# Optimization experiments

Hardware: AMD Instinct MI355X
Metric: run time of the kernel (lower is better)

The kernel has to match this reference:

```python
import jax, jax.numpy as jnp
import numpy as np

HEADS, DIM_HEAD, DIM = 12, 64, 768
H = W = 32
N = H * W
B = 4


def _ln(x, g, b, eps=1e-5):
    mu = x.mean(-1, keepdims=True)
    var = ((x - mu) ** 2).mean(-1, keepdims=True)
    return (x - mu) / jnp.sqrt(var + eps) * g + b


def _get_epipolar(k, src_c2w, target_c2w, h=H, w=W):
    # Faithful port of Epipolar_Attention.get_epipolar, without the (hw*hw,3) repeat
    # materialization (uses broadcasting for the pairwise cross product instead).
    b = k.shape[0]
    Wf = h * 16.0 / 9.0
    k = k.astype(jnp.float32)
    k = k.at[:, 0, :].multiply(Wf).at[:, 1, :].multiply(float(h))
    k = k.at[:, 0, 2].set(h / 2.0).at[:, 1, 2].set(h / 2.0)
    ii, jj = jnp.meshgrid(jnp.arange(h), jnp.arange(w), indexing='ij')
    # after the torch column swap: (col, row, 1)
    coords = jnp.stack([jj.ravel(), ii.ravel(), jnp.ones(h * w, jnp.int32)], axis=1).astype(jnp.float32)  # [hw,3]
    k3 = k[:, :3, :3]
    src_r, src_t = src_c2w[:, :3, :3].astype(jnp.float32), src_c2w[:, :3, 3].astype(jnp.float32)
    tgt_r, tgt_t = target_c2w[:, :3, :3].astype(jnp.float32), target_c2w[:, :3, 3].astype(jnp.float32)
    tgt_rinv = jnp.linalg.inv(tgt_r)
    fx, fy = k3[:, 0, 0][:, None], k3[:, 1, 1][:, None]
    cx, cy = k3[:, 0, 2][:, None], k3[:, 1, 2][:, None]
    nc = jnp.stack([(coords[None, :, 0] - cx) / fx,
                    (coords[None, :, 1] - cy) / fy,
                    jnp.broadcast_to(coords[None, :, 2], (b, h * w))], axis=-1)  # [b,hw,3]
    p3w = jnp.einsum('bij,bnj->bni', src_r, nc) + src_t[:, None]
    p2 = jnp.einsum('bij,bnj->bni', tgt_rinv, p3w) - tgt_t[:, None]  # target_w2c_t = -target_c2w_t
    pij_un = jnp.einsum('bij,bnj->bni', k3, p2)                      # [b,hw,3]
    pij = pij_un / (pij_un[..., -1:] + 1e-6)
    o2 = jnp.einsum('bij,bj->bi', tgt_rinv, src_t) - tgt_t           # origin projected
    oij = jnp.einsum('bij,bj->bi', k3, o2)
    oij = oij / oij[..., -1:]
    oi_to_pi = pij - oij[:, None]                # [b,hw,3]
    oi_to_coord = coords[None] - oij[:, None]    # [b,hw,3]
    cr = jnp.cross(oi_to_pi[:, :, None, :], oi_to_coord[:, None, :, :])  # [b,hw,hw,3]
    area = jnp.sqrt((cr * cr).sum(-1))
    vlen = jnp.sqrt((oi_to_pi * oi_to_pi).sum(-1))[:, :, None]
    dist = area / vlen
    dw = 1.0 - jax.nn.sigmoid(50.0 * (dist - 0.5))
    row_max = dw.max(-1, keepdims=True)
    return jnp.where(row_max < 0.5, 1.0, dw)     # rows with max<0.5 are set to all-ones


def setup_inputs():
    key = jax.random.key(0)
    ks = jax.random.split(key, 16)
    s = 0.02
    x = jax.random.normal(ks[0], (B, N, DIM), jnp.float32)
    src_encode = jax.random.normal(ks[1], (B, N, DIM), jnp.float32)
    intrinsic = (jnp.zeros((B, 4, 4), jnp.float32)
                 .at[:, 0, 0].set(1.0).at[:, 1, 1].set(1.0)
                 .at[:, 0, 2].set(0.5).at[:, 1, 2].set(0.5)
                 .at[:, 2, 2].set(1.0).at[:, 3, 3].set(1.0))
    R = jnp.eye(3, dtype=jnp.float32) + 0.1 * jax.random.normal(ks[2], (2, B, 3, 3), jnp.float32)
    t = 0.5 * jax.random.normal(ks[3], (2, B, 3), jnp.float32)
    c2w = (jnp.zeros((2, B, 4, 4), jnp.float32)
           .at[:, :, :3, :3].set(R).at[:, :, :3, 3].set(t).at[:, :, 3, 3].set(1.0))
    hd = HEADS * DIM_HEAD
    w_ = lambda k_, shp: s * jax.random.normal(k_, shp, jnp.float32)
    return dict(
        x=x, src_encode=src_encode, intrinsic=intrinsic, c2w=c2w,
        lnq_g=jnp.ones(DIM), lnq_b=jnp.zeros(DIM), Wq=w_(ks[4], (DIM, hd)), bq=jnp.zeros(hd),
        lnk_g=jnp.ones(DIM), lnk_b=jnp.zeros(DIM), Wk=w_(ks[5], (DIM, hd)), bk=jnp.zeros(hd),
        lnv_g=jnp.ones(DIM), lnv_b=jnp.zeros(DIM), Wv=w_(ks[6], (DIM, hd)), bv=jnp.zeros(hd),
        Wp=w_(ks[7], (hd, DIM)), bp=jnp.zeros(DIM),
        pre_g=jnp.ones(DIM), pre_b=jnp.zeros(DIM),
        W1=w_(ks[8], (DIM, 2 * DIM)), b1=jnp.zeros(2 * DIM),
        W2=w_(ks[9], (2 * DIM, DIM)), b2=jnp.zeros(DIM),
        post_g=jnp.ones(DIM), post_b=jnp.zeros(DIM))


def reference(x, src_encode, intrinsic, c2w, lnq_g, lnq_b, Wq, bq, lnk_g, lnk_b, Wk, bk,
              lnv_g, lnv_b, Wv, bv, Wp, bp, pre_g, pre_b, W1, b1, W2, b2, post_g, post_b):
    b, n, _ = x.shape
    scale = DIM_HEAD ** -0.5
    split = lambda t_: t_.reshape(b, n, HEADS, DIM_HEAD).transpose(0, 2, 1, 3)  # [b,m,n,d]
    q = split(_ln(x, lnq_g, lnq_b) @ Wq + bq)
    k = split(_ln(src_encode, lnk_g, lnk_b) @ Wk + bk)
    v = split(_ln(src_encode, lnv_g, lnv_b) @ Wv + bv)
    scores = scale * jnp.einsum('bmqd,bmkd->bmqk', q, k)
    e1 = _get_epipolar(intrinsic, c2w[1], c2w[0])                    # do_epipolar
    e2 = jnp.swapaxes(_get_epipolar(intrinsic, c2w[0], c2w[1]), 1, 2)  # bidirectional (transposed)
    wmap = e1 * e2                                                   # [b,n,n], shared across heads
    att = jax.nn.softmax(scores * wmap[:, None], axis=-1)
    a = jnp.einsum('bmqk,bmkd->bmqd', att, v).transpose(0, 2, 1, 3).reshape(b, n, HEADS * DIM_HEAD)
    z = _ln(a @ Wp + bp, pre_g, pre_b)
    z = z + (jax.nn.gelu(z @ W1 + b1, approximate=False) @ W2 + b2)  # torch nn.GELU = exact erf
    z = _ln(z, post_g, post_b)
    wm_full = jnp.broadcast_to(wmap[:, None], (b, HEADS, n, n)).reshape(b * HEADS, n, n)
    return z, wm_full
```

## Files before the change

kernel.cpp:

```cpp
#include <hip/hip_runtime.h>
#include <hip/hip_bf16.h>

typedef unsigned short u16;
typedef __attribute__((ext_vector_type(4))) unsigned short u16x4;
typedef __attribute__((ext_vector_type(8))) unsigned short u16x8;
typedef __attribute__((ext_vector_type(8))) short s16x8;
typedef __attribute__((ext_vector_type(4))) float f32x4;

#define HEADS 12
#define NSEQ 1024
#define DIMM 768
#define DHEAD 64

__device__ __forceinline__ float b2f(u16 h) {
  union { unsigned u; float f; } v; v.u = ((unsigned)h) << 16; return v.f;
}
__device__ __forceinline__ u16 f2b(float f) {
  union { float f; unsigned u; } v; v.f = f;
  unsigned r = v.u + 0x7fffu + ((v.u >> 16) & 1u);
  return (u16)(r >> 16);
}
__device__ __forceinline__ void gl_lds16(const u16* g, u16* l) {
  __builtin_amdgcn_global_load_lds(
      (const __attribute__((address_space(1))) void*)g,
      (__attribute__((address_space(3))) void*)l, 16, 0, 0);
}

template<bool GELU, bool RESID>
__device__ __forceinline__ void gemm_body(
    const u16* __restrict__ A, const u16* __restrict__ BT,
    const float* __restrict__ bias, const u16* __restrict__ resid,
    const float* __restrict__ rg, const float* __restrict__ rb,
    u16* __restrict__ C, int K, int lda, int ldb, int ldc,
    int m0, int n0, u16* As, u16* Bs)
{
  const int tid = threadIdx.x;
  const int lane = tid & 63;
  const int wv = tid >> 6;
  const int wm0 = (wv >> 1) * 64;
  const int wn0 = (wv & 1) * 64;
  const int l15 = lane & 15;
  const int quad = lane >> 4;
  const int srow = lane >> 2;
  const int scol = (lane & 3) * 8;

  f32x4 acc[4][4];
  #pragma unroll
  for (int i = 0; i < 4; ++i)
    #pragma unroll
    for (int j = 0; j < 4; ++j)
      acc[i][j] = {0.f, 0.f, 0.f, 0.f};

  const u16* Ab = A + (long)(m0 + wv * 32 + srow) * lda + scol;
  const u16* Bb = BT + (long)(n0 + wv * 32 + srow) * ldb + scol;
  u16* AsW = As + (wv * 32) * 32;
  u16* BsW = Bs + (wv * 32) * 32;

  #pragma unroll
  for (int t = 0; t < 2; ++t) {
    gl_lds16(Ab + (long)t * 16 * lda, AsW + t * 16 * 32);
    gl_lds16(Bb + (long)t * 16 * ldb, BsW + t * 16 * 32);
  }

  int cur = 0;
  for (int k0 = 0; k0 < K; k0 += 32) {
    __syncthreads();
    if (k0 + 32 < K) {
      const int nxt = cur ^ 1;
      #pragma unroll
      for (int t = 0; t < 2; ++t) {
        gl_lds16(Ab + (k0 + 32) + (long)t * 16 * lda, AsW + nxt * 4096 + t * 16 * 32);
        gl_lds16(Bb + (k0 + 32) + (long)t * 16 * ldb, BsW + nxt * 4096 + t * 16 * 32);
      }
    }
    const u16* Ac = As + cur * 4096;
    const u16* Bc = Bs + cur * 4096;
    s16x8 af[4], bfr[4];
    #pragma unroll
    for (int i = 0; i < 4; ++i)
      af[i] = *(const s16x8*)&Ac[(wm0 + i * 16 + l15) * 32 + quad * 8];
    #pragma unroll
    for (int j = 0; j < 4; ++j)
      bfr[j] = *(const s16x8*)&Bc[(wn0 + j * 16 + l15) * 32 + quad * 8];
    #pragma unroll
    for (int i = 0; i < 4; ++i)
      #pragma unroll
      for (int j = 0; j < 4; ++j)
        acc[i][j] = __builtin_amdgcn_mfma_f32_16x16x32_bf16(af[i], bfr[j], acc[i][j], 0, 0, 0);
    cur ^= 1;
  }

  #pragma unroll
  for (int i = 0; i < 4; ++i)
    #pragma unroll
    for (int j = 0; j < 4; ++j) {
      const int col = n0 + wn0 + j * 16 + l15;
      const float bvv = bias[col];
      #pragma unroll
      for (int v = 0; v < 4; ++v) {
        const int row = m0 + wm0 + i * 16 + quad * 4 + v;
        float val = acc[i][j][v] + bvv;
        if (GELU) val = 0.5f * val * (1.0f + erff(val * 0.70710678118654752440f));
        if (RESID) val += b2f(resid[(long)row * ldc + col]) * rg[col] + rb[col];
        C[(long)row * ldc + col] = f2b(val);
      }
    }
}

template<bool GELU, bool RESID>
__device__ __forceinline__ void gemm_body64(
    const u16* __restrict__ A, const u16* __restrict__ BT,
    const float* __restrict__ bias, const u16* __restrict__ resid,
    const float* __restrict__ rg, const float* __restrict__ rb,
    u16* __restrict__ C, int K, int lda, int ldb, int ldc,
    int m0, int n0, u16* As, u16* Bs)
{
  const int tid = threadIdx.x;
  const int lane = tid & 63;
  const int wv = tid >> 6;
  const int wm0 = wv * 32;
  const int l15 = lane & 15;
  const int quad = lane >> 4;
  const int srow = lane >> 2;
  const int scol = (lane & 3) * 8;

  f32x4 acc[2][4];
  #pragma unroll
  for (int i = 0; i < 2; ++i)
    #pragma unroll
    for (int j = 0; j < 4; ++j)
      acc[i][j] = {0.f, 0.f, 0.f, 0.f};

  const u16* Ab = A + (long)(m0 + wv * 32 + srow) * lda + scol;
  const u16* Bb = BT + (long)(n0 + wv * 16 + srow) * ldb + scol;
  u16* AsW = As + (wv * 32) * 32;
  u16* BsW = Bs + (wv * 16) * 32;

  #pragma unroll
  for (int t = 0; t < 2; ++t)
    gl_lds16(Ab + (long)t * 16 * lda, AsW + t * 16 * 32);
  gl_lds16(Bb, BsW);

  int cur = 0;
  for (int k0 = 0; k0 < K; k0 += 32) {
    __syncthreads();
    if (k0 + 32 < K) {
      const int nxt = cur ^ 1;
      #pragma unroll
      for (int t = 0; t < 2; ++t)
        gl_lds16(Ab + (k0 + 32) + (long)t * 16 * lda, AsW + nxt * 4096 + t * 16 * 32);
      gl_lds16(Bb + (k0 + 32), BsW + nxt * 2048);
    }
    const u16* Ac = As + cur * 4096;
    const u16* Bc = Bs + cur * 2048;
    s16x8 af[2], bfr[4];
    #pragma unroll
    for (int i = 0; i < 2; ++i)
      af[i] = *(const s16x8*)&Ac[(wm0 + i * 16 + l15) * 32 + quad * 8];
    #pragma unroll
    for (int j = 0; j < 4; ++j)
      bfr[j] = *(const s16x8*)&Bc[(j * 16 + l15) * 32 + quad * 8];
    #pragma unroll
    for (int i = 0; i < 2; ++i)
      #pragma unroll
      for (int j = 0; j < 4; ++j)
        acc[i][j] = __builtin_amdgcn_mfma_f32_16x16x32_bf16(af[i], bfr[j], acc[i][j], 0, 0, 0);
    cur ^= 1;
  }

  #pragma unroll
  for (int i = 0; i < 2; ++i)
    #pragma unroll
    for (int j = 0; j < 4; ++j) {
      const int col = n0 + j * 16 + l15;
      const float bvv = bias[col];
      #pragma unroll
      for (int v = 0; v < 4; ++v) {
        const int row = m0 + wm0 + i * 16 + quad * 4 + v;
        float val = acc[i][j][v] + bvv;
        if (GELU) val = 0.5f * val * (1.0f + erff(val * 0.70710678118654752440f));
        if (RESID) val += b2f(resid[(long)row * ldc + col]) * rg[col] + rb[col];
        C[(long)row * ldc + col] = f2b(val);
      }
    }
}

template<bool GELU, bool RESID>
__global__ __launch_bounds__(256)
void gemm_one(const u16* __restrict__ A, const u16* __restrict__ BT,
              const float* __restrict__ bias, const u16* __restrict__ resid,
              const float* __restrict__ rg, const float* __restrict__ rb,
              u16* __restrict__ C, int K, int lda, int ldb, int ldc)
{
  __shared__ u16 As[8192], Bs[4096];
  gemm_body64<GELU, RESID>(A, BT, bias, resid, rg, rb, C, K, lda, ldb, ldc,
                           blockIdx.x * 128, blockIdx.y * 64, As, Bs);
}

__global__ __launch_bounds__(256)
void gemm_qkv(const u16* __restrict__ nx, const u16* __restrict__ ns,
              const u16* __restrict__ qT, const u16* __restrict__ kvT,
              const float* __restrict__ bqf, const float* __restrict__ bkvf,
              u16* __restrict__ qb, u16* __restrict__ kvb)
{
  __shared__ u16 As[8192], Bs[8192];
  const int z = blockIdx.z;
  if (z == 0)
    gemm_body<false, false>(nx, qT, bqf, nullptr, nullptr, nullptr, qb,
                            768, 768, 768, 768,
                            blockIdx.x * 128, blockIdx.y * 128, As, Bs);
  else
    gemm_body<false, false>(ns, kvT, bkvf, nullptr, nullptr, nullptr, kvb,
                            768, 768, 768, 1536,
                            blockIdx.x * 128, (z - 1) * 768 + blockIdx.y * 128, As, Bs);
}

__global__ __launch_bounds__(256, 3)
void fattn(const u16* __restrict__ qb, const u16* __restrict__ kvb,
           const u16* __restrict__ vT, const u16* __restrict__ wm,
           u16* __restrict__ outA)
{
  __shared__ u16 Qs[2 * 64 * 32];
  __shared__ u16 Ks[2][2 * 64 * 32];
  __shared__ u16 Vs[2][2 * 64 * 32];
  __shared__ u16 Ps[64][72];

  const int bh = blockIdx.y;
  const int b = bh / HEADS, h = bh - b * HEADS;
  const int q0 = blockIdx.x * 64;
  const int tid = threadIdx.x;
  const int lane = tid & 63;
  const int wv = tid >> 6;
  const int l15 = lane & 15;
  const int quad = lane >> 4;
  const int srow = lane >> 2;
  const int scol = (lane & 3) * 8;

  const u16* Qg = qb + ((long)b * NSEQ + q0) * DIMM + h * DHEAD;
  const u16* Kg = kvb + (long)b * NSEQ * 1536 + h * DHEAD;
  const u16* Vg = vT + (long)bh * DHEAD * NSEQ;
  const u16* Wg = wm + ((long)b * NSEQ + q0) * NSEQ;

  #pragma unroll
  for (int h2 = 0; h2 < 2; ++h2) {
    gl_lds16(Qg + (long)(wv * 16 + srow) * DIMM + h2 * 32 + scol,
             Qs + (h2 * 64 + wv * 16) * 32);
    gl_lds16(Kg + (long)(wv * 16 + srow) * 1536 + h2 * 32 + scol,
             Ks[0] + (h2 * 64 + wv * 16) * 32);
    gl_lds16(Vg + (long)(wv * 16 + srow) * NSEQ + h2 * 32 + scol,
             Vs[0] + (h2 * 64 + wv * 16) * 32);
  }

  f32x4 Sacc[4], Oacc[4];
  float mrow[4], lrow[4];
  #pragma unroll
  for (int j = 0; j < 4; ++j) {
    Oacc[j] = {0.f, 0.f, 0.f, 0.f};
    mrow[j] = -3.0e38f;
    lrow[j] = 0.f;
  }
  s16x8 qf[2];

  int cur = 0;
  for (int kt = 0; kt < 16; ++kt) {
    __syncthreads();
    if (kt < 15) {
      const int nxt = cur ^ 1;
      #pragma unroll
      for (int h2 = 0; h2 < 2; ++h2) {
        gl_lds16(Kg + (long)((kt + 1) * 64 + wv * 16 + srow) * 1536 + h2 * 32 + scol,
                 Ks[nxt] + (h2 * 64 + wv * 16) * 32);
        gl_lds16(Vg + (long)(wv * 16 + srow) * NSEQ + (kt + 1) * 64 + h2 * 32 + scol,
                 Vs[nxt] + (h2 * 64 + wv * 16) * 32);
      }
    }

    if (kt == 0) {
      qf[0] = *(const s16x8*)&Qs[(0 * 64 + wv * 16 + l15) * 32 + quad * 8];
      qf[1] = *(const s16x8*)&Qs[(1 * 64 + wv * 16 + l15) * 32 + quad * 8];
    }

    float wr[4][4];
    #pragma unroll
    for (int j = 0; j < 4; ++j)
      #pragma unroll
      for (int v = 0; v < 4; ++v)
        wr[j][v] = b2f(Wg[(long)(wv * 16 + quad * 4 + v) * NSEQ + kt * 64 + j * 16 + l15]);

    #pragma unroll
    for (int j = 0; j < 4; ++j) Sacc[j] = {0.f, 0.f, 0.f, 0.f};
    #pragma unroll
    for (int j = 0; j < 4; ++j)
      #pragma unroll
      for (int h2 = 0; h2 < 2; ++h2) {
        s16x8 kf = *(const s16x8*)&Ks[cur][(h2 * 64 + j * 16 + l15) * 32 + quad * 8];
        Sacc[j] = __builtin_amdgcn_mfma_f32_16x16x32_bf16(qf[h2], kf, Sacc[j], 0, 0, 0);
      }

    #pragma unroll
    for (int j = 0; j < 4; ++j)
      #pragma unroll
      for (int v = 0; v < 4; ++v)
        Sacc[j][v] *= wr[j][v];
    #pragma unroll
    for (int v = 0; v < 4; ++v) {
      float tm = fmaxf(fmaxf(Sacc[0][v], Sacc[1][v]), fmaxf(Sacc[2][v], Sacc[3][v]));
      tm = fmaxf(tm, __shfl_xor(tm, 1));
      tm = fmaxf(tm, __shfl_xor(tm, 2));
      tm = fmaxf(tm, __shfl_xor(tm, 4));
      tm = fmaxf(tm, __shfl_xor(tm, 8));
      const float mnew = fmaxf(mrow[v], tm);
      const float al = __expf(mrow[v] - mnew);
      float rs = 0.f;
      #pragma unroll
      for (int j = 0; j < 4; ++j) {
        const float e = __expf(Sacc[j][v] - mnew);
        Sacc[j][v] = e;
        rs += e;
      }
      rs += __shfl_xor(rs, 1);
      rs += __shfl_xor(rs, 2);
      rs += __shfl_xor(rs, 4);
      rs += __shfl_xor(rs, 8);
      lrow[v] = lrow[v] * al + rs;
      mrow[v] = mnew;
      #pragma unroll
      for (int jn = 0; jn < 4; ++jn) Oacc[jn][v] *= al;
    }
    #pragma unroll
    for (int j = 0; j < 4; ++j)
      #pragma unroll
      for (int v = 0; v < 4; ++v)
        Ps[wv * 16 + quad * 4 + v][j * 16 + l15] = f2b(Sacc[j][v]);

    #pragma unroll
    for (int h2 = 0; h2 < 2; ++h2) {
      s16x8 af = *(const s16x8*)&Ps[wv * 16 + l15][h2 * 32 + quad * 8];
      #pragma unroll
      for (int jn = 0; jn < 4; ++jn) {
        s16x8 vf = *(const s16x8*)&Vs[cur][(h2 * 64 + jn * 16 + l15) * 32 + quad * 8];
        Oacc[jn] = __builtin_amdgcn_mfma_f32_16x16x32_bf16(af, vf, Oacc[jn], 0, 0, 0);
      }
    }
    cur ^= 1;
  }

  #pragma unroll
  for (int v = 0; v < 4; ++v) {
    const int row = q0 + wv * 16 + quad * 4 + v;
    const float inv = 1.0f / lrow[v];
    #pragma unroll
    for (int jn = 0; jn < 4; ++jn)
      outA[((long)(b * NSEQ + row)) * DIMM + h * DHEAD + jn * 16 + l15] =
          f2b(Oacc[jn][v] * inv);
  }
}

template<bool F32IN>
__global__ __launch_bounds__(256)
void norm_k(const void* __restrict__ in, u16* __restrict__ out)
{
  const long base = (long)blockIdx.x * DIMM;
  const int tid = threadIdx.x;
  __shared__ float s1[8], s2[8];
  float v0, v1, v2;
  if (F32IN) {
    const float* p = (const float*)in + base;
    v0 = p[tid]; v1 = p[tid + 256]; v2 = p[tid + 512];
  } else {
    const u16* p = (const u16*)in + base;
    v0 = b2f(p[tid]); v1 = b2f(p[tid + 256]); v2 = b2f(p[tid + 512]);
  }
  float s = v0 + v1 + v2;
  #pragma unroll
  for (int off = 32; off; off >>= 1) s += __shfl_down(s, off);
  const int lane = tid & 63, wid = tid >> 6;
  if (!lane) s1[wid] = s;
  __syncthreads();
  if (!tid) s1[4] = s1[0] + s1[1] + s1[2] + s1[3];
  __syncthreads();
  const float mu = s1[4] / 768.0f;
  float d0 = v0 - mu, d1 = v1 - mu, d2 = v2 - mu;
  float sq = d0 * d0 + d1 * d1 + d2 * d2;
  #pragma unroll
  for (int off = 32; off; off >>= 1) sq += __shfl_down(sq, off);
  if (!lane) s2[wid] = sq;
  __syncthreads();
  if (!tid) s2[4] = s2[0] + s2[1] + s2[2] + s2[3];
  __syncthreads();
  const float rstd = 1.0f / sqrtf(s2[4] / 768.0f + 1e-5f);
  u16* o = out + base;
  o[tid]       = f2b(d0 * rstd);
  o[tid + 256] = f2b(d1 * rstd);
  o[tid + 512] = f2b(d2 * rstd);
}

__global__ __launch_bounds__(256)
void norm_dual(const float* __restrict__ inA, const float* __restrict__ inB,
               u16* __restrict__ outA, u16* __restrict__ outB)
{
  const int r = blockIdx.x;
  const float* p = ((r < 4096) ? inA : inB) + (long)(r & 4095) * DIMM;
  u16* o = ((r < 4096) ? outA : outB) + (long)(r & 4095) * DIMM;
  const int tid = threadIdx.x;
  __shared__ float s1[8], s2[8];
  float v0 = p[tid], v1 = p[tid + 256], v2 = p[tid + 512];
  float s = v0 + v1 + v2;
  #pragma unroll
  for (int off = 32; off; off >>= 1) s += __shfl_down(s, off);
  const int lane = tid & 63, wid = tid >> 6;
  if (!lane) s1[wid] = s;
  __syncthreads();
  if (!tid) s1[4] = s1[0] + s1[1] + s1[2] + s1[3];
  __syncthreads();
  const float mu = s1[4] / 768.0f;
  float d0 = v0 - mu, d1 = v1 - mu, d2 = v2 - mu;
  float sq = d0 * d0 + d1 * d1 + d2 * d2;
  #pragma unroll
  for (int off = 32; off; off >>= 1) sq += __shfl_down(sq, off);
  if (!lane) s2[wid] = sq;
  __syncthreads();
  if (!tid) s2[4] = s2[0] + s2[1] + s2[2] + s2[3];
  __syncthreads();
  const float rstd = 1.0f / sqrtf(s2[4] / 768.0f + 1e-5f);
  o[tid]       = f2b(d0 * rstd);
  o[tid + 256] = f2b(d1 * rstd);
  o[tid + 512] = f2b(d2 * rstd);
}

__global__ __launch_bounds__(256)
void ln_final(const u16* __restrict__ in, const float* __restrict__ g,
              const float* __restrict__ bb, float* __restrict__ out)
{
  const long base = (long)blockIdx.x * DIMM;
  const int tid = threadIdx.x;
  __shared__ float s1[8], s2[8];
  const u16* p = in + base;
  float v0 = b2f(p[tid]), v1 = b2f(p[tid + 256]), v2 = b2f(p[tid + 512]);
  float s = v0 + v1 + v2;
  #pragma unroll
  for (int off = 32; off; off >>= 1) s += __shfl_down(s, off);
  const int lane = tid & 63, wid = tid >> 6;
  if (!lane) s1[wid] = s;
  __syncthreads();
  if (!tid) s1[4] = s1[0] + s1[1] + s1[2] + s1[3];
  __syncthreads();
  const float mu = s1[4] / 768.0f;
  float d0 = v0 - mu, d1 = v1 - mu, d2 = v2 - mu;
  float sq = d0 * d0 + d1 * d1 + d2 * d2;
  #pragma unroll
  for (int off = 32; off; off >>= 1) sq += __shfl_down(sq, off);
  if (!lane) s2[wid] = sq;
  __syncthreads();
  if (!tid) s2[4] = s2[0] + s2[1] + s2[2] + s2[3];
  __syncthreads();
  const float rstd = 1.0f / sqrtf(s2[4] / 768.0f + 1e-5f);
  float* o = out + base;
  o[tid]       = d0 * rstd * g[tid]       + bb[tid];
  o[tid + 256] = d1 * rstd * g[tid + 256] + bb[tid + 256];
  o[tid + 512] = d2 * rstd * g[tid + 512] + bb[tid + 512];
}

__global__ __launch_bounds__(256)
void trans_all(const float* w0, const float* w1, const float* w2,
               const float* w3, const float* w4, const float* w5,
               const float* gq, const float* gk, const float* gv, const float* gp,
               u16* d0, u16* d12, u16* d3, u16* d4, u16* d5)
{
  const float* src; const float* g; u16* dst; int R, C; float sc = 1.0f;
  switch (blockIdx.z) {
    case 0: src = w0; g = gq; dst = d0;  R = 768;  C = 768;  sc = 0.125f; break;
    case 1: src = w1; g = gk; dst = d12; R = 768;  C = 768;  break;
    case 2: src = w2; g = gv; dst = d12 + 768 * 768; R = 768; C = 768; break;
    case 3: src = w3; g = nullptr; dst = d3; R = 768;  C = 768;  break;
    case 4: src = w4; g = gp; dst = d4; R = 768;  C = 1536; break;
    default: src = w5; g = nullptr; dst = d5; R = 1536; C = 768; break;
  }
  const int c0 = blockIdx.x * 32;
  const int r0 = blockIdx.y * 32;
  if (c0 >= C || r0 >= R) return;
  __shared__ u16 t[32][36];
  const int tid = threadIdx.x;
  const int i = tid >> 3;
  const int j4 = (tid & 7) * 4;
  const float rs = (g ? g[r0 + i] : 1.0f) * sc;
  #pragma unroll
  for (int jj = 0; jj < 4; ++jj)
    t[i][j4 + jj] = f2b(src[(long)(r0 + i) * C + c0 + j4 + jj] * rs);
  __syncthreads();
  u16x4 ov;
  #pragma unroll
  for (int jj = 0; jj < 4; ++jj) ov[jj] = t[j4 + jj][i];
  *(u16x4*)&dst[(long)(c0 + i) * R + r0 + j4] = ov;
}

__global__ __launch_bounds__(256)
void biasfold(const float* Wq, const float* Wk, const float* Wv, const float* W1,
              const float* bq, const float* bk, const float* bv, const float* b1,
              const float* lnqb, const float* lnkb, const float* lnvb, const float* preb,
              float* obq, float* obkv, float* ob1)
{
  const int y = blockIdx.y;
  const int c = blockIdx.x * 256 + threadIdx.x;
  const float* W; const float* bln; const float* bw; float* out;
  int C; float sc = 1.0f;
  switch (y) {
    case 0: W = Wq; bln = lnqb; bw = bq; out = obq;        C = 768;  sc = 0.125f; break;
    case 1: W = Wk; bln = lnkb; bw = bk; out = obkv;       C = 768;  break;
    case 2: W = Wv; bln = lnvb; bw = bv; out = obkv + 768; C = 768;  break;
    default: W = W1; bln = preb; bw = b1; out = ob1;       C = 1536; break;
  }
  if (c >= C) return;
  float s = bw[c];
  for (int r = 0; r < 768; ++r) s += bln[r] * W[(long)r * C + c];
  out[c] = s * sc;
}

__global__ __launch_bounds__(256)
void v_transpose(const u16* __restrict__ kvb, u16* __restrict__ vT)
{
  __shared__ u16 t[64][72];
  const int z = blockIdx.y;
  const int b = z / HEADS, h = z - b * HEADS;
  const int n0 = blockIdx.x * 64;
  const int tid = threadIdx.x;
  const int i = tid >> 2;
  const int jb = (tid & 3) * 16;
  const u16* src = kvb + (long)(b * NSEQ + n0 + i) * 1536 + 768 + h * DHEAD + jb;
  *(u16x8*)&t[i][jb]     = *(const u16x8*)&src[0];
  *(u16x8*)&t[i][jb + 8] = *(const u16x8*)&src[8];
  __syncthreads();
  const int dd = tid >> 2;
  const int nb = (tid & 3) * 16;
  u16x8 o0, o1;
  #pragma unroll
  for (int nn = 0; nn < 8; ++nn) { o0[nn] = t[nb + nn][dd]; o1[nn] = t[nb + 8 + nn][dd]; }
  u16* dst = vT + ((long)z * DHEAD + dd) * NSEQ + n0 + nb;
  *(u16x8*)&dst[0] = o0;
  *(u16x8*)&dst[8] = o1;
}

__global__ void epi_setup(const float* __restrict__ intr, const float* __restrict__ c2w,
                          float* __restrict__ u4, float* __restrict__ oijb)
{
  const int db = blockIdx.x;
  const int d = db >> 2, b = db & 3;
  __shared__ float S[36];
  if (threadIdx.x == 0) {
    const int sidx = (d == 0) ? 1 : 0;
    const int tidx = 1 - sidx;
    float k3[9], sr[9], st[3], tr[9], tt[3];
    const float Wf = 32.0f * 16.0f / 9.0f;
    for (int j = 0; j < 3; ++j) {
      k3[j]     = intr[(b * 4 + 0) * 4 + j] * Wf;
      k3[3 + j] = intr[(b * 4 + 1) * 4 + j] * 32.0f;
      k3[6 + j] = intr[(b * 4 + 2) * 4 + j];
    }
    k3[2] = 16.0f; k3[5] = 16.0f;
    for (int i = 0; i < 3; ++i) {
      for (int j = 0; j < 3; ++j) {
        sr[i * 3 + j] = c2w[((sidx * 4 + b) * 4 + i) * 4 + j];
        tr[i * 3 + j] = c2w[((tidx * 4 + b) * 4 + i) * 4 + j];
      }
      st[i] = c2w[((sidx * 4 + b) * 4 + i) * 4 + 3];
      tt[i] = c2w[((tidx * 4 + b) * 4 + i) * 4 + 3];
    }
    double a = tr[0], bb_ = tr[1], c = tr[2];
    double dd2 = tr[3], e = tr[4], f = tr[5];
    double g2 = tr[6], h2 = tr[7], i2 = tr[8];
    double det = a * (e * i2 - f * h2) - bb_ * (dd2 * i2 - f * g2) + c * (dd2 * h2 - e * g2);
    double inv[9] = {
      (e * i2 - f * h2), (c * h2 - bb_ * i2), (bb_ * f - c * e),
      (f * g2 - dd2 * i2), (a * i2 - c * g2), (c * dd2 - a * f),
      (dd2 * h2 - e * g2), (bb_ * g2 - a * h2), (a * e - bb_ * dd2)
    };
    float tri[9];
    for (int t2 = 0; t2 < 9; ++t2) tri[t2] = (float)(inv[t2] / det);
    float o2[3], oij[3];
    for (int i3 = 0; i3 < 3; ++i3)
      o2[i3] = tri[i3 * 3] * st[0] + tri[i3 * 3 + 1] * st[1] + tri[i3 * 3 + 2] * st[2] - tt[i3];
    for (int i3 = 0; i3 < 3; ++i3)
      oij[i3] = k3[i3 * 3] * o2[0] + k3[i3 * 3 + 1] * o2[1] + k3[i3 * 3 + 2] * o2[2];
    const float ozf = oij[2];
    oij[0] = oij[0] / ozf; oij[1] = oij[1] / ozf; oij[2] = ozf / ozf;
    for (int t2 = 0; t2 < 9; ++t2) { S[t2] = k3[t2]; S[9 + t2] = sr[t2]; S[21 + t2] = tri[t2]; }
    for (int t2 = 0; t2 < 3; ++t2) { S[18 + t2] = st[t2]; S[30 + t2] = tt[t2]; S[33 + t2] = oij[t2]; }
    oijb[db * 4 + 0] = oij[0]; oijb[db * 4 + 1] = oij[1]; oijb[db * 4 + 2] = oij[2];
    oijb[db * 4 + 3] = 0.f;
  }
  __syncthreads();
  for (int n = threadIdx.x; n < 1024; n += blockDim.x) {
    const float ncx = ((float)(n & 31) - S[2]) / S[0];
    const float ncy = ((float)(n >> 5) - S[5]) / S[4];
    const float p0 = S[9]  * ncx + S[10] * ncy + S[11] + S[18];
    const float p1 = S[12] * ncx + S[13] * ncy + S[14] + S[19];
    const float p2 = S[15] * ncx + S[16] * ncy + S[17] + S[20];
    const float q0 = S[21] * p0 + S[22] * p1 + S[23] * p2 - S[30];
    const float q1 = S[24] * p0 + S[25] * p1 + S[26] * p2 - S[31];
    const float q2 = S[27] * p0 + S[28] * p1 + S[29] * p2 - S[32];
    const float w0 = S[0] * q0 + S[1] * q1 + S[2] * q2;
    const float w1 = S[3] * q0 + S[4] * q1 + S[5] * q2;
    const float w2 = S[6] * q0 + S[7] * q1 + S[8] * q2;
    const float pz = w2 + 1e-6f;
    const float ux = w0 / pz - S[33];
    const float uy = w1 / pz - S[34];
    const float uz = w2 / pz - S[35];
    const float vlen = sqrtf(ux * ux + uy * uy + uz * uz);
    f32x4 uo = {ux, uy, uz, vlen};
    *(f32x4*)&u4[((long)db * 1024 + n) * 4] = uo;
  }
}

__device__ __forceinline__ float dwval(f32x4 U, float ox, float oy, float oz, int m)
{
  const float cx = (float)(m & 31) - ox;
  const float cy = (float)(m >> 5) - oy;
  const float cz = 1.0f - oz;
  const float crx = U.y * cz - U.z * cy;
  const float cry = U.z * cx - U.x * cz;
  const float crz = U.x * cy - U.y * cx;
  const float area = sqrtf(crx * crx + cry * cry + crz * crz);
  const float dist = area / U.w;
  const float t = 50.0f * (dist - 0.5f);
  return 1.0f - 1.0f / (1.0f + __expf(-t));
}

__global__ __launch_bounds__(256)
void epi_flags(const float* __restrict__ u4, const float* __restrict__ oijb,
               float* __restrict__ flags)
{
  const int rowid = blockIdx.x;
  const int db = rowid >> 10;
  const f32x4 U = *(const f32x4*)&u4[(long)rowid * 4];
  const float ox = oijb[db * 4 + 0];
  const float oy = oijb[db * 4 + 1];
  const float oz = oijb[db * 4 + 2];
  const int tid = threadIdx.x;
  __shared__ float red[8];
  float mx = -1e30f;
  #pragma unroll
  for (int i = 0; i < 4; ++i)
    mx = fmaxf(mx, dwval(U, ox, oy, oz, tid + i * 256));
  #pragma unroll
  for (int off = 32; off; off >>= 1) mx = fmaxf(mx, __shfl_down(mx, off));
  const int lane = tid & 63, wid = tid >> 6;
  if (!lane) red[wid] = mx;
  __syncthreads();
  if (!tid) {
    const float m4 = fmaxf(fmaxf(red[0], red[1]), fmaxf(red[2], red[3]));
    flags[rowid] = (m4 < 0.5f) ? 1.0f : 0.0f;
  }
}

__global__ __launch_bounds__(256)
void epi_wmap(const float* __restrict__ u4, const float* __restrict__ oijb,
              const float* __restrict__ flags,
              u16* __restrict__ wm, float* __restrict__ wm_full)
{
  const int b = blockIdx.z;
  const int q0 = blockIdx.x * 32;
  const int k0 = blockIdx.y * 32;
  const int tid = threadIdx.x;
  const int i = tid >> 3;
  const int j4 = (tid & 7) * 4;

  __shared__ f32x4 U2s[32];
  __shared__ float f2s[32];
  __shared__ float f1s[32];
  if (tid < 32) {
    U2s[tid] = *(const f32x4*)&u4[((long)(4 + b) * 1024 + k0 + tid) * 4];
    f2s[tid] = flags[(4 + b) * 1024 + k0 + tid];
    f1s[tid] = flags[b * 1024 + q0 + tid];
  }
  __syncthreads();

  const int q = q0 + i;
  const f32x4 U1 = *(const f32x4*)&u4[((long)b * 1024 + q) * 4];
  const float o1x = oijb[b * 4 + 0], o1y = oijb[b * 4 + 1], o1z = oijb[b * 4 + 2];
  const float o2x = oijb[(4 + b) * 4 + 0], o2y = oijb[(4 + b) * 4 + 1], o2z = oijb[(4 + b) * 4 + 2];
  const bool fl1 = f1s[i] > 0.5f;

  u16x4 pk;
  f32x4 wf;
  #pragma unroll
  for (int jj = 0; jj < 4; ++jj) {
    const int k = k0 + j4 + jj;
    const float e1 = fl1 ? 1.0f : dwval(U1, o1x, o1y, o1z, k);
    const float e2 = (f2s[j4 + jj] > 0.5f) ? 1.0f : dwval(U2s[j4 + jj], o2x, o2y, o2z, q);
    const float w = e1 * e2;
    wf[jj] = w;
    pk[jj] = f2b(w);
  }
  *(u16x4*)&wm[((long)b * 1024 + q0 + i) * 1024 + k0 + j4] = pk;
  #pragma unroll
  for (int h = 0; h < HEADS; ++h)
    *(f32x4*)&wm_full[((long)(b * HEADS + h) * 1024 + q0 + i) * 1024 + k0 + j4] = wf;
}

extern "C" void kernel_launch(void* const* d_in, const int* in_sizes, int n_in,
                              void* d_out, int out_size, void* d_ws, size_t ws_size,
                              hipStream_t stream)
{
  (void)in_sizes; (void)n_in; (void)out_size; (void)ws_size;
  const float* x     = (const float*)d_in[0];
  const float* src   = (const float*)d_in[1];
  const float* intr  = (const float*)d_in[2];
  const float* c2w   = (const float*)d_in[3];
  const float* lnq_g = (const float*)d_in[4];
  const float* lnq_b = (const float*)d_in[5];
  const float* Wq    = (const float*)d_in[6];
  const float* bq    = (const float*)d_in[7];
  const float* lnk_g = (const float*)d_in[8];
  const float* lnk_b = (const float*)d_in[9];
  const float* Wk    = (const float*)d_in[10];
  const float* bk    = (const float*)d_in[11];
  const float* lnv_g = (const float*)d_in[12];
  const float* lnv_b = (const float*)d_in[13];
  const float* Wv    = (const float*)d_in[14];
  const float* bv    = (const float*)d_in[15];
  const float* Wp    = (const float*)d_in[16];
  const float* bp    = (const float*)d_in[17];
  const float* pre_g = (const float*)d_in[18];
  const float* pre_b = (const float*)d_in[19];
  const float* W1    = (const float*)d_in[20];
  const float* b1    = (const float*)d_in[21];
  const float* W2    = (const float*)d_in[22];
  const float* b2    = (const float*)d_in[23];
  const float* post_g= (const float*)d_in[24];
  const float* post_b= (const float*)d_in[25];

  char* ws = (char*)d_ws;
  size_t off = 0;
  auto alloc = [&](size_t bytes) -> char* {
    char* p = ws + off;
    off = (off + bytes + 255) & ~(size_t)255;
    return p;
  };
  const size_t SEQD = (size_t)4096 * 768 * 2;

  u16* WqT  = (u16*)alloc(768 * 768 * 2);
  u16* WkvT = (u16*)alloc((size_t)1536 * 768 * 2);
  u16* WpT  = (u16*)alloc(768 * 768 * 2);
  u16* W1T  = (u16*)alloc(768 * 1536 * 2);
  u16* W2T  = (u16*)alloc(1536 * 768 * 2);
  float* bqf  = (float*)alloc(768 * 4);
  float* bkvf = (float*)alloc(1536 * 4);
  float* b1f  = (float*)alloc(1536 * 4);
  char* pool = alloc(6 * SEQD);
  float* u4   = (float*)alloc(8 * 1024 * 4 * 4);
  float* oijb = (float*)alloc(8 * 4 * 4);
  u16* wmapb  = (u16*)alloc((size_t)4 * 1024 * 1024 * 2);
  float* flagb = (float*)alloc(8 * 1024 * 4);

  u16* S0 = (u16*)pool;
  u16* S1 = (u16*)(pool + SEQD);
  u16* S2 = (u16*)(pool + 2 * SEQD);
  u16* S3 = (u16*)(pool + 3 * SEQD);
  u16* S5 = (u16*)(pool + 5 * SEQD);

  float* out_z  = (float*)d_out;
  float* out_wm = (float*)d_out + (size_t)4 * 1024 * 768;

  trans_all<<<dim3(48, 48, 6), 256, 0, stream>>>(
      Wq, Wk, Wv, Wp, W1, W2, lnq_g, lnk_g, lnv_g, pre_g,
      WqT, WkvT, WpT, W1T, W2T);
  biasfold<<<dim3(6, 4), 256, 0, stream>>>(
      Wq, Wk, Wv, W1, bq, bk, bv, b1, lnq_b, lnk_b, lnv_b, pre_b,
      bqf, bkvf, b1f);

  epi_setup<<<8, 128, 0, stream>>>(intr, c2w, u4, oijb);
  epi_flags<<<8192, 256, 0, stream>>>(u4, oijb, flagb);
  epi_wmap<<<dim3(32, 32, 4), 256, 0, stream>>>(u4, oijb, flagb, wmapb, out_wm);

  norm_dual<<<8192, 256, 0, stream>>>(x, src, S0, S1);

  gemm_qkv<<<dim3(32, 6, 3), 256, 0, stream>>>(S0, S1, WqT, WkvT, bqf, bkvf, S2, S3);

  v_transpose<<<dim3(16, 48), 256, 0, stream>>>(S3, S5);

  fattn<<<dim3(16, 48), 256, 0, stream>>>(S2, S3, S5, wmapb, S0);

  gemm_one<false, false><<<dim3(32, 12), 256, 0, stream>>>(
      S0, WpT, bp, nullptr, nullptr, nullptr, S1, 768, 768, 768, 768);

  norm_k<false><<<4096, 256, 0, stream>>>(S1, S2);

  gemm_one<true, false><<<dim3(32, 24), 256, 0, stream>>>(
      S2, W1T, b1f, nullptr, nullptr, nullptr, S3, 768, 768, 768, 1536);

  gemm_one<false, true><<<dim3(32, 12), 256, 0, stream>>>(
      S3, W2T, b2, S2, pre_g, pre_b, S5, 1536, 1536, 1536, 768);

  ln_final<<<4096, 256, 0, stream>>>(S5, post_g, post_b, out_z);
}
```

Measured before the change: 518.7 us.

## Triple-buffer GEMM LDS loads with vmcnt waits and fuse biasfold into weight prep

Both GEMM bodies move from double to triple buffering of LDS tiles filled by direct global-to-LDS loads. Each iteration waits with explicit s_waitcnt vmcnt counts and a raw barrier instead of __syncthreads, so two tiles stay in flight and load latency is hidden better. Separately, the bias-folding kernel is merged into the weight transpose kernel as an extra z-slice, with the 768-row reduction split over 8 thread groups, removing one launch and widening that reduction. The change raises LDS per block and depends on the hand-written vmcnt values matching the number of outstanding loads.

After: 511.5 us. About the same (-1.4%).

```diff
diff --git a/kernel.cpp b/kernel.cpp
--- a/kernel.cpp
+++ b/kernel.cpp
@@ -56,38 +56,43 @@
   u16* AsW = As + (wv * 32) * 32;
   u16* BsW = Bs + (wv * 32) * 32;
 
-  #pragma unroll
-  for (int t = 0; t < 2; ++t) {
-    gl_lds16(Ab + (long)t * 16 * lda, AsW + t * 16 * 32);
-    gl_lds16(Bb + (long)t * 16 * ldb, BsW + t * 16 * 32);
-  }
+  auto issue = [&](int buf, int kk) {
+    #pragma unroll
+    for (int t = 0; t < 2; ++t) {
+      gl_lds16(Ab + kk + (long)t * 16 * lda, AsW + buf * 4096 + t * 16 * 32);
+      gl_lds16(Bb + kk + (long)t * 16 * ldb, BsW + buf * 4096 + t * 16 * 32);
+    }
+  };
+
+  const int NK = K >> 5;
+  issue(0, 0);
+  issue(1, 32);
 
   int cur = 0;
-  for (int k0 = 0; k0 < K; k0 += 32) {
-    __syncthreads();
-    if (k0 + 32 < K) {
-      const int nxt = cur ^ 1;
-      #pragma unroll
-      for (int t = 0; t < 2; ++t) {
-        gl_lds16(Ab + (k0 + 32) + (long)t * 16 * lda, AsW + nxt * 4096 + t * 16 * 32);
-        gl_lds16(Bb + (k0 + 32) + (long)t * 16 * ldb, BsW + nxt * 4096 + t * 16 * 32);
-      }
+  for (int i = 0; i < NK; ++i) {
+    if (i + 1 < NK) asm volatile("s_waitcnt vmcnt(4)" ::: "memory");
+    else            asm volatile("s_waitcnt vmcnt(0)" ::: "memory");
+    __builtin_amdgcn_s_barrier();
+    __builtin_amdgcn_sched_barrier(0);
+    if (i + 2 < NK) {
+      int nb = cur + 2; if (nb >= 3) nb -= 3;
+      issue(nb, (i + 2) * 32);
     }
     const u16* Ac = As + cur * 4096;
     const u16* Bc = Bs + cur * 4096;
     s16x8 af[4], bfr[4];
     #pragma unroll
-    for (int i = 0; i < 4; ++i)
-      af[i] = *(const s16x8*)&Ac[(wm0 + i * 16 + l15) * 32 + quad * 8];
+    for (int i2 = 0; i2 < 4; ++i2)
+      af[i2] = *(const s16x8*)&Ac[(wm0 + i2 * 16 + l15) * 32 + quad * 8];
     #pragma unroll
     for (int j = 0; j < 4; ++j)
       bfr[j] = *(const s16x8*)&Bc[(wn0 + j * 16 + l15) * 32 + quad * 8];
     #pragma unroll
-    for (int i = 0; i < 4; ++i)
+    for (int i2 = 0; i2 < 4; ++i2)
       #pragma unroll
       for (int j = 0; j < 4; ++j)
-        acc[i][j] = __builtin_amdgcn_mfma_f32_16x16x32_bf16(af[i], bfr[j], acc[i][j], 0, 0, 0);
-    cur ^= 1;
+        acc[i2][j] = __builtin_amdgcn_mfma_f32_16x16x32_bf16(af[i2], bfr[j], acc[i2][j], 0, 0, 0);
+    ++cur; if (cur == 3) cur = 0;
   }
 
   #pragma unroll
@@ -136,36 +141,42 @@
   u16* AsW = As + (wv * 32) * 32;
   u16* BsW = Bs + (wv * 16) * 32;
 
-  #pragma unroll
-  for (int t = 0; t < 2; ++t)
-    gl_lds16(Ab + (long)t * 16 * lda, AsW + t * 16 * 32);
-  gl_lds16(Bb, BsW);
+  auto issue = [&](int buf, int kk) {
+    #pragma unroll
+    for (int t = 0; t < 2; ++t)
+      gl_lds16(Ab + kk + (long)t * 16 * lda, AsW + buf * 4096 + t * 16 * 32);
+    gl_lds16(Bb + kk, BsW + buf * 2048);
+  };
+
+  const int NK = K >> 5;
+  issue(0, 0);
+  issue(1, 32);
 
   int cur = 0;
-  for (int k0 = 0; k0 < K; k0 += 32) {
-    __syncthreads();
-    if (k0 + 32 < K) {
-      const int nxt = cur ^ 1;
-      #pragma unroll
-      for (int t = 0; t < 2; ++t)
-        gl_lds16(Ab + (k0 + 32) + (long)t * 16 * lda, AsW + nxt * 4096 + t * 16 * 32);
-      gl_lds16(Bb + (k0 + 32), BsW + nxt * 2048);
+  for (int i = 0; i < NK; ++i) {
+    if (i + 1 < NK) asm volatile("s_waitcnt vmcnt(3)" ::: "memory");
+    else            asm volatile("s_waitcnt vmcnt(0)" ::: "memory");
+    __builtin_amdgcn_s_barrier();
+    __builtin_amdgcn_sched_barrier(0);
+    if (i + 2 < NK) {
+      int nb = cur + 2; if (nb >= 3) nb -= 3;
+      issue(nb, (i + 2) * 32);
     }
     const u16* Ac = As + cur * 4096;
     const u16* Bc = Bs + cur * 2048;
     s16x8 af[2], bfr[4];
     #pragma unroll
-    for (int i = 0; i < 2; ++i)
-      af[i] = *(const s16x8*)&Ac[(wm0 + i * 16 + l15) * 32 + quad * 8];
+    for (int i2 = 0; i2 < 2; ++i2)
+      af[i2] = *(const s16x8*)&Ac[(wm0 + i2 * 16 + l15) * 32 + quad * 8];
     #pragma unroll
     for (int j = 0; j < 4; ++j)
       bfr[j] = *(const s16x8*)&Bc[(j * 16 + l15) * 32 + quad * 8];
     #pragma unroll
-    for (int i = 0; i < 2; ++i)
+    for (int i2 = 0; i2 < 2; ++i2)
       #pragma unroll
       for (int j = 0; j < 4; ++j)
-        acc[i][j] = __builtin_amdgcn_mfma_f32_16x16x32_bf16(af[i], bfr[j], acc[i][j], 0, 0, 0);
-    cur ^= 1;
+        acc[i2][j] = __builtin_amdgcn_mfma_f32_16x16x32_bf16(af[i2], bfr[j], acc[i2][j], 0, 0, 0);
+    ++cur; if (cur == 3) cur = 0;
   }
 
   #pragma unroll
@@ -192,7 +203,7 @@
               const float* __restrict__ rg, const float* __restrict__ rb,
               u16* __restrict__ C, int K, int lda, int ldb, int ldc)
 {
-  __shared__ u16 As[8192], Bs[4096];
+  __shared__ u16 As[12288], Bs[6144];
   gemm_body64<GELU, RESID>(A, BT, bias, resid, rg, rb, C, K, lda, ldb, ldc,
                            blockIdx.x * 128, blockIdx.y * 64, As, Bs);
 }
@@ -203,7 +214,7 @@
               const float* __restrict__ bqf, const float* __restrict__ bkvf,
               u16* __restrict__ qb, u16* __restrict__ kvb)
 {
-  __shared__ u16 As[8192], Bs[8192];
+  __shared__ u16 As[12288], Bs[12288];
   const int z = blockIdx.z;
   if (z == 0)
     gemm_body<false, false>(nx, qT, bqf, nullptr, nullptr, nullptr, qb,
@@ -462,11 +473,48 @@
 }
 
 __global__ __launch_bounds__(256)
-void trans_all(const float* w0, const float* w1, const float* w2,
-               const float* w3, const float* w4, const float* w5,
-               const float* gq, const float* gk, const float* gv, const float* gp,
-               u16* d0, u16* d12, u16* d3, u16* d4, u16* d5)
-{
+void prep_all(const float* w0, const float* w1, const float* w2,
+              const float* w3, const float* w4, const float* w5,
+              const float* gq, const float* gk, const float* gv, const float* gp,
+              u16* d0, u16* d12, u16* d3, u16* d4, u16* d5,
+              const float* bq, const float* bk, const float* bv, const float* b1,
+              const float* lnqb, const float* lnkb, const float* lnvb, const float* preb,
+              float* obq, float* obkv, float* ob1)
+{
+  __shared__ u16 t[32][36];
+  __shared__ float red[8][32];
+  const int tid = threadIdx.x;
+
+  if (blockIdx.z == 6) {
+    const int y = blockIdx.y;
+    if (y >= 4) return;
+    const float* W; const float* bln; const float* bw; float* out;
+    int C; float sc = 1.0f;
+    switch (y) {
+      case 0: W = w0; bln = lnqb; bw = bq; out = obq;        C = 768;  sc = 0.125f; break;
+      case 1: W = w1; bln = lnkb; bw = bk; out = obkv;       C = 768;  break;
+      case 2: W = w2; bln = lnvb; bw = bv; out = obkv + 768; C = 768;  break;
+      default: W = w4; bln = preb; bw = b1; out = ob1;       C = 1536; break;
+    }
+    const int c0 = blockIdx.x * 32;
+    if (c0 >= C) return;
+    const int cl = tid & 31;
+    const int rg = tid >> 5;
+    const int c = c0 + cl;
+    float s = 0.f;
+    for (int r = rg * 96; r < rg * 96 + 96; ++r)
+      s += bln[r] * W[(long)r * C + c];
+    red[rg][cl] = s;
+    __syncthreads();
+    if (rg == 0) {
+      float tot = bw[c];
+      #pragma unroll
+      for (int k = 0; k < 8; ++k) tot += red[k][cl];
+      out[c] = tot * sc;
+    }
+    return;
+  }
+
   const float* src; const float* g; u16* dst; int R, C; float sc = 1.0f;
   switch (blockIdx.z) {
     case 0: src = w0; g = gq; dst = d0;  R = 768;  C = 768;  sc = 0.125f; break;
@@ -479,8 +527,6 @@
   const int c0 = blockIdx.x * 32;
   const int r0 = blockIdx.y * 32;
   if (c0 >= C || r0 >= R) return;
-  __shared__ u16 t[32][36];
-  const int tid = threadIdx.x;
   const int i = tid >> 3;
   const int j4 = (tid & 7) * 4;
   const float rs = (g ? g[r0 + i] : 1.0f) * sc;
@@ -492,28 +538,6 @@
   #pragma unroll
   for (int jj = 0; jj < 4; ++jj) ov[jj] = t[j4 + jj][i];
   *(u16x4*)&dst[(long)(c0 + i) * R + r0 + j4] = ov;
-}
-
-__global__ __launch_bounds__(256)
-void biasfold(const float* Wq, const float* Wk, const float* Wv, const float* W1,
-              const float* bq, const float* bk, const float* bv, const float* b1,
-              const float* lnqb, const float* lnkb, const float* lnvb, const float* preb,
-              float* obq, float* obkv, float* ob1)
-{
-  const int y = blockIdx.y;
-  const int c = blockIdx.x * 256 + threadIdx.x;
-  const float* W; const float* bln; const float* bw; float* out;
-  int C; float sc = 1.0f;
-  switch (y) {
-    case 0: W = Wq; bln = lnqb; bw = bq; out = obq;        C = 768;  sc = 0.125f; break;
-    case 1: W = Wk; bln = lnkb; bw = bk; out = obkv;       C = 768;  break;
-    case 2: W = Wv; bln = lnvb; bw = bv; out = obkv + 768; C = 768;  break;
-    default: W = W1; bln = preb; bw = b1; out = ob1;       C = 1536; break;
-  }
-  if (c >= C) return;
-  float s = bw[c];
-  for (int r = 0; r < 768; ++r) s += bln[r] * W[(long)r * C + c];
-  out[c] = s * sc;
 }
 
 __global__ __launch_bounds__(256)
@@ -761,11 +785,10 @@
   float* out_z  = (float*)d_out;
   float* out_wm = (float*)d_out + (size_t)4 * 1024 * 768;
 
-  trans_all<<<dim3(48, 48, 6), 256, 0, stream>>>(
+  prep_all<<<dim3(48, 48, 7), 256, 0, stream>>>(
       Wq, Wk, Wv, Wp, W1, W2, lnq_g, lnk_g, lnv_g, pre_g,
-      WqT, WkvT, WpT, W1T, W2T);
-  biasfold<<<dim3(6, 4), 256, 0, stream>>>(
-      Wq, Wk, Wv, W1, bq, bk, bv, b1, lnq_b, lnk_b, lnv_b, pre_b,
+      WqT, WkvT, WpT, W1T, W2T,
+      bq, bk, bv, b1, lnq_b, lnk_b, lnv_b, pre_b,
       bqf, bkvf, b1f);
 
   epi_setup<<<8, 128, 0, stream>>>(intr, c2w, u4, oijb);
```
